# Kernel tuning notes

Hardware: AMD Instinct MI355X
Metric: run time of the kernel (lower is better)

The kernel has to match this reference:

```python
import jax, jax.numpy as jnp
import numpy as np

V, E, H = 348, 512, 1024  # vocab, embed dim, GRU hidden


def gru_cell(x, h, w_ih, w_hh, b_ih, b_hh):
    # PyTorch GRUCell: gates ordered [r, z, n] along the 3H axis
    gi = x @ w_ih.T + b_ih            # [B, 3H]
    gh = h @ w_hh.T + b_hh            # [B, 3H]
    i_r, i_z, i_n = jnp.split(gi, 3, axis=-1)
    h_r, h_z, h_n = jnp.split(gh, 3, axis=-1)
    r = jax.nn.sigmoid(i_r + h_r)
    z = jax.nn.sigmoid(i_z + h_z)
    n = jnp.tanh(i_n + r * h_n)
    return (1.0 - z) * n + z * h


def setup_inputs() -> dict:
    key = jax.random.key(0)
    ks = jax.random.split(key, 20)
    B, T = 256, 128
    p = lambda k, shape: jax.random.normal(k, shape, dtype=jnp.float32) * 0.02
    return {
        "target": jax.random.randint(ks[0], (B, T), 0, V, dtype=jnp.int32),
        "bos": 1,
        "emb": p(ks[1], (V, E)),
        "w_ih1": p(ks[2], (3 * H, E)),  "w_hh1": p(ks[3], (3 * H, H)),
        "b_ih1": p(ks[4], (3 * H,)),    "b_hh1": p(ks[5], (3 * H,)),
        "w_ih2": p(ks[6], (3 * H, H)),  "w_hh2": p(ks[7], (3 * H, H)),
        "b_ih2": p(ks[8], (3 * H,)),    "b_hh2": p(ks[9], (3 * H,)),
        "w_ih3": p(ks[10], (3 * H, H)), "w_hh3": p(ks[11], (3 * H, H)),
        "b_ih3": p(ks[12], (3 * H,)),   "b_hh3": p(ks[13], (3 * H,)),
        "w_out": p(ks[14], (V, H)),     "b_out": p(ks[15], (V,)),
    }


def reference(target, bos, emb, w_ih1, w_hh1, b_ih1, b_hh1,
              w_ih2, w_hh2, b_ih2, b_hh2,
              w_ih3, w_hh3, b_ih3, b_hh3, w_out, b_out):
    B, T = target.shape
    # input tokens = [<bos>, target[:, :-1]]
    x_in = jnp.concatenate(
        [jnp.full((B, 1), bos, dtype=target.dtype), target[:, :-1]], axis=1)
    h0 = jnp.zeros((B, H), jnp.float32)
    lp0 = jnp.zeros((B,), jnp.float32)

    def step(carry, xt):
        h1, h2, h3, lp = carry
        tok, tgt = xt                     # [B], [B]
        e = emb[tok]                      # [B, E]
        h1 = gru_cell(e, h1, w_ih1, w_hh1, b_ih1, b_hh1)
        h2 = gru_cell(h1, h2, w_ih2, w_hh2, b_ih2, b_hh2)
        h3 = gru_cell(h2, h3, w_ih3, w_hh3, b_ih3, b_hh3)
        logits = h3 @ w_out.T + b_out     # [B, V]
        logp = jax.nn.log_softmax(logits, axis=-1)
        # NLLLoss in source = sum(one_hot(tgt) * log_prob) = gathered log-prob
        lp = lp + jnp.take_along_axis(logp, tgt[:, None], axis=1)[:, 0]
        return (h1, h2, h3, lp), None

    (_, _, _, log_probs), _ = jax.lax.scan(
        step, (h0, h0, h0, lp0), (x_in.T, target.T))
    return log_probs
```

## Files before the change

### kernel.cpp

```cpp
#include <hip/hip_runtime.h>
#include <hip/hip_bf16.h>
#include <cstdint>

constexpr int kT = 128;
constexpr int kB = 256;
constexpr int kE = 512;
constexpr int kH = 1024;
constexpr int kV = 348;
constexpr int kNG = 3072;
constexpr int NB = 208;

constexpr float kScale = 32.f;
constexpr float kInvSS = 1.f / 1024.f;

typedef float f4v __attribute__((ext_vector_type(4)));
typedef unsigned short u16;
typedef unsigned char u8;

__device__ __forceinline__ u8 f2e4m3(float x) {
  int p = __builtin_amdgcn_cvt_pk_fp8_f32(x, x, 0, false);
  return (u8)(p & 0xff);
}

__device__ __forceinline__ uint64_t ldv_u64(const void* p) {
  return __hip_atomic_load((const uint64_t*)p, __ATOMIC_RELAXED, __HIP_MEMORY_SCOPE_AGENT);
}
__device__ __forceinline__ void stv_u8(u8* p, u8 v) {
  __hip_atomic_store(p, v, __ATOMIC_RELAXED, __HIP_MEMORY_SCOPE_AGENT);
}

__device__ __forceinline__ int permn(int n) {
  int gate = n >> 10, j = n & 1023;
  return ((j >> 4) * 48) + gate * 16 + (j & 15);
}

struct Params {
  const int* target; const int* bosp; const float* b_out;
  const u8 *w1i, *w1h, *w2i, *w2h, *w3i, *w3h, *wout, *embb;
  const float *bi1, *bh1, *bi2, *bh2, *bi3, *bh3;
  float *h1f, *h2f, *h3f;
  u8    *h1b, *h2b, *h3b;
  float *lp;
  unsigned *acnt; unsigned *gflag;
};

union SMem {
  struct { u8 A[128 * 128]; u8 B[96 * 128]; } mm;
  float logits[16 * 400];
};

__device__ __forceinline__ void gbar(unsigned* acnt, unsigned* gflag, unsigned s) {
  asm volatile("s_waitcnt vmcnt(0)" ::: "memory");
  __syncthreads();
  if (threadIdx.x == 0) {
    const unsigned g = blockIdx.x & 31u;
    __hip_atomic_fetch_add(&acnt[g * 16], 1u, __ATOMIC_RELAXED, __HIP_MEMORY_SCOPE_AGENT);
    if (blockIdx.x == 0) {
      for (;;) {
        unsigned sum = 0;
#pragma unroll
        for (int i = 0; i < 32; ++i)
          sum += __hip_atomic_load(&acnt[i * 16], __ATOMIC_RELAXED, __HIP_MEMORY_SCOPE_AGENT);
        if (sum >= (unsigned)NB * (s + 1u)) break;
        __builtin_amdgcn_s_sleep(4);
      }
#pragma unroll
      for (int i = 0; i < 32; ++i)
        __hip_atomic_store(&gflag[i * 16], s + 1u, __ATOMIC_RELAXED, __HIP_MEMORY_SCOPE_AGENT);
    } else {
      while (__hip_atomic_load(&gflag[g * 16], __ATOMIC_RELAXED, __HIP_MEMORY_SCOPE_AGENT) <= s)
        __builtin_amdgcn_s_sleep(8);
    }
    asm volatile("" ::: "memory");
  }
  __syncthreads();
}

template<int K, bool EMB>
__device__ __forceinline__ void mm_phase(SMem& sm, const u8* __restrict__ Asrc,
    const u8* __restrict__ W, int b0, int n0,
    f4v* aR, f4v* aZ, f4v* aN,
    const int* __restrict__ target, int bos, int u)
{
  const int t = threadIdx.x, lane = t & 63, wv = t >> 6;
  const int wm = wv >> 1, wg = wv & 1, li = lane & 15, q = lane >> 4;
  uint64_t ra[4][2];
  uint4 rb[3];

  auto stage = [&](int k0) {
#pragma unroll
    for (int p = 0; p < 4; ++p) {
      int id = p * 256 + t, r = id >> 3, c = id & 7;
      if (EMB) {
        int tok = (u == 0) ? bos : target[(b0 + r) * kT + (u - 1)];
        uint4 v = *(const uint4*)&Asrc[(size_t)tok * K + k0 + c * 16];
        ra[p][0] = ((uint64_t)v.y << 32) | v.x;
        ra[p][1] = ((uint64_t)v.w << 32) | v.z;
      } else {
        const u8* src = Asrc + (size_t)(b0 + r) * kH + k0 + c * 16;
        ra[p][0] = ldv_u64(src); ra[p][1] = ldv_u64(src + 8);
      }
    }
#pragma unroll
    for (int p = 0; p < 3; ++p) {
      int id = p * 256 + t, r = id >> 3, c = id & 7;
      rb[p] = *(const uint4*)&W[(size_t)(n0 + r) * K + k0 + c * 16];
    }
  };

  stage(0);
  for (int it = 0; it < K / 128; ++it) {
    __syncthreads();
#pragma unroll
    for (int p = 0; p < 4; ++p) {
      int id = p * 256 + t, r = id >> 3, c = id & 7;
      const int u0 = c * 2, rx = r & 15;
      u8* base = &sm.mm.A[r * 128];
      *(uint64_t*)(base + 8 * (u0 ^ rx)) = ra[p][0];
      *(uint64_t*)(base + 8 * ((u0 + 1) ^ rx)) = ra[p][1];
    }
#pragma unroll
    for (int p = 0; p < 3; ++p) {
      int id = p * 256 + t, r = id >> 3, c = id & 7;
      const int u0 = c * 2, rx = r & 15;
      u8* base = &sm.mm.B[r * 128];
      *(uint64_t*)(base + 8 * (u0 ^ rx)) = (uint64_t)rb[p].x | ((uint64_t)rb[p].y << 32);
      *(uint64_t*)(base + 8 * ((u0 + 1) ^ rx)) = (uint64_t)rb[p].z | ((uint64_t)rb[p].w << 32);
    }
    __syncthreads();
    if (it + 1 < K / 128) stage((it + 1) * 128);
#pragma unroll
    for (int kk = 0; kk < 128; kk += 32) {
      const int swz = 8 * (((kk >> 3) + q) ^ li);
      long a[4], bb[3];
#pragma unroll
      for (int m2 = 0; m2 < 4; ++m2)
        a[m2] = *(const long*)&sm.mm.A[(64 * wm + 16 * m2 + li) * 128 + swz];
#pragma unroll
      for (int g = 0; g < 3; ++g)
        bb[g] = *(const long*)&sm.mm.B[(48 * wg + 16 * g + li) * 128 + swz];
#pragma unroll
      for (int m2 = 0; m2 < 4; ++m2) {
        aR[m2] = __builtin_amdgcn_mfma_f32_16x16x32_fp8_fp8(a[m2], bb[0], aR[m2], 0, 0, 0);
        aZ[m2] = __builtin_amdgcn_mfma_f32_16x16x32_fp8_fp8(a[m2], bb[1], aZ[m2], 0, 0, 0);
        aN[m2] = __builtin_amdgcn_mfma_f32_16x16x32_fp8_fp8(a[m2], bb[2], aN[m2], 0, 0, 0);
      }
    }
  }
}

template<int K1, bool L1>
__device__ void do_L(SMem& sm, const u8* __restrict__ xsrc,
                     const u8* __restrict__ hbPrev, const float* __restrict__ hfPrev,
                     const u8* __restrict__ Wih, const u8* __restrict__ Whh,
                     const float* __restrict__ biP, const float* __restrict__ bhP,
                     float* __restrict__ hfOut, u8* __restrict__ hbOut,
                     const int* __restrict__ target, int bos, int u, int mt, int jt)
{
  const int b0 = mt * 128, j0 = jt * 32, n0 = jt * 96;
  f4v aR[4], aZ[4], aNi[4], aNh[4];
#pragma unroll
  for (int i = 0; i < 4; ++i) {
    aR[i] = f4v{0.f,0.f,0.f,0.f}; aZ[i] = f4v{0.f,0.f,0.f,0.f};
    aNi[i] = f4v{0.f,0.f,0.f,0.f}; aNh[i] = f4v{0.f,0.f,0.f,0.f};
  }
  mm_phase<K1, L1>(sm, xsrc, Wih, b0, n0, aR, aZ, aNi, target, bos, u);
  mm_phase<kH, false>(sm, hbPrev, Whh, b0, n0, aR, aZ, aNh, target, bos, u);

  const int t = threadIdx.x, lane = t & 63, wv = t >> 6;
  const int wm = wv >> 1, wg = wv & 1, li = lane & 15, q = lane >> 4;
  const int j = j0 + 16 * wg + li;
  const int cr = n0 + 48 * wg + li;
  const float bR = biP[cr] + bhP[cr];
  const float bZ = biP[cr + 16] + bhP[cr + 16];
  const float biN = biP[cr + 32], bhN = bhP[cr + 32];
  float hold[4][4];
#pragma unroll
  for (int m2 = 0; m2 < 4; ++m2)
#pragma unroll
    for (int r = 0; r < 4; ++r) {
      int b = b0 + 64 * wm + 16 * m2 + 4 * q + r;
      hold[m2][r] = hfPrev[(size_t)b * kH + j];
    }
#pragma unroll
  for (int m2 = 0; m2 < 4; ++m2)
#pragma unroll
    for (int r = 0; r < 4; ++r) {
      int b = b0 + 64 * wm + 16 * m2 + 4 * q + r;
      float rg = 1.f / (1.f + __expf(-(aR[m2][r] * kInvSS + bR)));
      float zg = 1.f / (1.f + __expf(-(aZ[m2][r] * kInvSS + bZ)));
      float np = (aNi[m2][r] * kInvSS + biN) + rg * (aNh[m2][r] * kInvSS + bhN);
      float nh = 2.f / (1.f + __expf(-2.f * np)) - 1.f;
      float hnew = (1.f - zg) * nh + zg * hold[m2][r];
      hfOut[(size_t)b * kH + j] = hnew;
      stv_u8(&hbOut[(size_t)b * kH + j], f2e4m3(hnew * kScale));
    }
}

__device__ void do_E(SMem& sm, const u8* __restrict__ h3b, const u8* __restrict__ wo,
                     const float* __restrict__ b_out, const int* __restrict__ target,
                     float* __restrict__ lp, int u, int tile)
{
  const int b0 = tile * 16;
  const int t = threadIdx.x, lane = t & 63, wv = t >> 6;
  const int li = lane & 15, q = lane >> 4;
  f4v acc[6];
#pragma unroll
  for (int f = 0; f < 6; ++f) acc[f] = f4v{0.f, 0.f, 0.f, 0.f};

  const u8* ap = h3b + (size_t)(b0 + li) * kH + q * 8;
  uint64_t aCur = ldv_u64(ap);
  uint64_t bCur[6], bNx[6];
#pragma unroll
  for (int f = 0; f < 6; ++f)
    bCur[f] = *(const uint64_t*)&wo[(size_t)(96 * wv + 16 * f + li) * kH + q * 8];
  for (int k0 = 0; k0 < kH; k0 += 32) {
    uint64_t aNx = 0;
    if (k0 + 32 < kH) {
      aNx = ldv_u64(ap + k0 + 32);
#pragma unroll
      for (int f = 0; f < 6; ++f)
        bNx[f] = *(const uint64_t*)&wo[(size_t)(96 * wv + 16 * f + li) * kH + k0 + 32 + q * 8];
    }
#pragma unroll
    for (int f = 0; f < 6; ++f)
      acc[f] = __builtin_amdgcn_mfma_f32_16x16x32_fp8_fp8((long)aCur, (long)bCur[f], acc[f], 0, 0, 0);
    aCur = aNx;
#pragma unroll
    for (int f = 0; f < 6; ++f) bCur[f] = bNx[f];
  }
#pragma unroll
  for (int f = 0; f < 6; ++f) {
    int n = 96 * wv + 16 * f + li;
    if (n < kV) {
      float bo = b_out[n];
#pragma unroll
      for (int r = 0; r < 4; ++r)
        sm.logits[(4 * q + r) * 400 + n] = acc[f][r] * kInvSS + bo;
    }
  }
  __syncthreads();
  int m = 4 * wv + q;
  int b = b0 + m;
  float mx = -1e30f;
  for (int cc = li; cc < kV; cc += 16) mx = fmaxf(mx, sm.logits[m * 400 + cc]);
#pragma unroll
  for (int d = 1; d < 16; d <<= 1) mx = fmaxf(mx, __shfl_xor(mx, d, 16));
  float se = 0.f;
  for (int cc = li; cc < kV; cc += 16) se += __expf(sm.logits[m * 400 + cc] - mx);
#pragma unroll
  for (int d = 1; d < 16; d <<= 1) se += __shfl_xor(se, d, 16);
  int tgt = target[b * kT + u];
  float logp = sm.logits[m * 400 + tgt] - mx - __logf(se);
  if (li == 0) lp[b] += logp;
}

__global__ __launch_bounds__(256, 1) void rnn_main(Params P)
{
  __shared__ SMem sm;
  const int bid = blockIdx.x;
  const int bos = P.bosp[0];
  const size_t HS = (size_t)kB * kH;

  const int local = bid & 63;
  const int mt = (local >> 3) & 1;
  const int jt = (local & 7) | ((local >> 4) << 3);

  for (int s = 0; s < kT + 3; ++s) {
    if (bid < 64) {
      int u = s;
      if (u < kT)
        do_L<kE, true>(sm, P.embb,
                       P.h1b + (size_t)((u - 1) & 1) * HS, P.h1f + (size_t)((u - 1) & 1) * HS,
                       P.w1i, P.w1h, P.bi1, P.bh1,
                       P.h1f + (size_t)(u & 1) * HS, P.h1b + (size_t)(u & 1) * HS,
                       P.target, bos, u, mt, jt);
    } else if (bid < 128) {
      int u = s - 1;
      if (u >= 0 && u < kT)
        do_L<kH, false>(sm, P.h1b + (size_t)(u & 1) * HS,
                        P.h2b + (size_t)((u - 1) & 1) * HS, P.h2f + (size_t)((u - 1) & 1) * HS,
                        P.w2i, P.w2h, P.bi2, P.bh2,
                        P.h2f + (size_t)(u & 1) * HS, P.h2b + (size_t)(u & 1) * HS,
                        P.target, bos, u, mt, jt);
    } else if (bid < 192) {
      int u = s - 2;
      if (u >= 0 && u < kT)
        do_L<kH, false>(sm, P.h2b + (size_t)(u & 1) * HS,
                        P.h3b + (size_t)((u - 1) & 1) * HS, P.h3f + (size_t)((u - 1) & 1) * HS,
                        P.w3i, P.w3h, P.bi3, P.bh3,
                        P.h3f + (size_t)(u & 1) * HS, P.h3b + (size_t)(u & 1) * HS,
                        P.target, bos, u, mt, jt);
    } else {
      int u = s - 3;
      if (u >= 0 && u < kT)
        do_E(sm, P.h3b + (size_t)(u & 1) * HS, P.wout, P.b_out, P.target, P.lp, u, bid - 192);
    }
    gbar(P.acnt, P.gflag, (unsigned)s);
  }
}

__global__ void k_conv_w(const float* __restrict__ w, u8* __restrict__ wp, int K, int logK) {
  int idx = blockIdx.x * 256 + threadIdx.x;
  if (idx >= kNG * K) return;
  int n = idx >> logK, k = idx & (K - 1);
  wp[(size_t)permn(n) * K + k] = f2e4m3(w[idx] * kScale);
}
__global__ void k_conv_b(const float* __restrict__ b, float* __restrict__ bp) {
  int idx = blockIdx.x * 256 + threadIdx.x;
  if (idx < kNG) bp[permn(idx)] = b[idx];
}
__global__ void k_conv_wout(const float* __restrict__ w, u8* __restrict__ wp) {
  int idx = blockIdx.x * 256 + threadIdx.x;
  if (idx >= 384 * kH) return;
  int n = idx >> 10, k = idx & 1023;
  wp[idx] = (n < kV) ? f2e4m3(w[(size_t)n * kH + k] * kScale) : (u8)0;
}
__global__ void k_conv_emb(const float* __restrict__ e, u8* __restrict__ ep) {
  int idx = blockIdx.x * 256 + threadIdx.x;
  if (idx < kV * kE) ep[idx] = f2e4m3(e[idx] * kScale);
}

extern "C" void kernel_launch(void* const* d_in, const int* in_sizes, int n_in,
                              void* d_out, int out_size, void* d_ws, size_t ws_size,
                              hipStream_t stream)
{
  const int*   target = (const int*)d_in[0];
  const int*   bosp   = (const int*)d_in[1];
  const float* emb    = (const float*)d_in[2];
  const float* w_ih1  = (const float*)d_in[3];
  const float* w_hh1  = (const float*)d_in[4];
  const float* b_ih1  = (const float*)d_in[5];
  const float* b_hh1  = (const float*)d_in[6];
  const float* w_ih2  = (const float*)d_in[7];
  const float* w_hh2  = (const float*)d_in[8];
  const float* b_ih2  = (const float*)d_in[9];
  const float* b_hh2  = (const float*)d_in[10];
  const float* w_ih3  = (const float*)d_in[11];
  const float* w_hh3  = (const float*)d_in[12];
  const float* b_ih3  = (const float*)d_in[13];
  const float* b_hh3  = (const float*)d_in[14];
  const float* w_out  = (const float*)d_in[15];
  const float* b_out  = (const float*)d_in[16];

  char* ws = (char*)d_ws;
  size_t off = 0;
  auto alloc = [&](size_t bytes) -> void* {
    void* p = ws + off;
    off = (off + bytes + 511) & ~(size_t)511;
    return p;
  };
  u8* w1i = (u8*)alloc((size_t)kNG * kE);
  u8* w1h = (u8*)alloc((size_t)kNG * kH);
  u8* w2i = (u8*)alloc((size_t)kNG * kH);
  u8* w2h = (u8*)alloc((size_t)kNG * kH);
  u8* w3i = (u8*)alloc((size_t)kNG * kH);
  u8* w3h = (u8*)alloc((size_t)kNG * kH);
  u8* wo  = (u8*)alloc((size_t)384 * kH);
  u8* eb  = (u8*)alloc((size_t)kV * kE);
  float* bi1 = (float*)alloc(kNG * 4);
  float* bh1 = (float*)alloc(kNG * 4);
  float* bi2 = (float*)alloc(kNG * 4);
  float* bh2 = (float*)alloc(kNG * 4);
  float* bi3 = (float*)alloc(kNG * 4);
  float* bh3 = (float*)alloc(kNG * 4);
  float* h1f = (float*)alloc((size_t)2 * kB * kH * 4);
  float* h2f = (float*)alloc((size_t)2 * kB * kH * 4);
  float* h3f = (float*)alloc((size_t)2 * kB * kH * 4);
  u8* h1b = (u8*)alloc((size_t)2 * kB * kH);
  u8* h2b = (u8*)alloc((size_t)2 * kB * kH);
  u8* h3b = (u8*)alloc((size_t)2 * kB * kH);
  unsigned* bar = (unsigned*)alloc(4096);
  (void)ws_size; (void)in_sizes; (void)n_in; (void)out_size;

  k_conv_w<<<(kNG * kE + 255) / 256, 256, 0, stream>>>(w_ih1, w1i, kE, 9);
  k_conv_w<<<(kNG * kH + 255) / 256, 256, 0, stream>>>(w_hh1, w1h, kH, 10);
  k_conv_w<<<(kNG * kH + 255) / 256, 256, 0, stream>>>(w_ih2, w2i, kH, 10);
  k_conv_w<<<(kNG * kH + 255) / 256, 256, 0, stream>>>(w_hh2, w2h, kH, 10);
  k_conv_w<<<(kNG * kH + 255) / 256, 256, 0, stream>>>(w_ih3, w3i, kH, 10);
  k_conv_w<<<(kNG * kH + 255) / 256, 256, 0, stream>>>(w_hh3, w3h, kH, 10);
  k_conv_b<<<(kNG + 255) / 256, 256, 0, stream>>>(b_ih1, bi1);
  k_conv_b<<<(kNG + 255) / 256, 256, 0, stream>>>(b_hh1, bh1);
  k_conv_b<<<(kNG + 255) / 256, 256, 0, stream>>>(b_ih2, bi2);
  k_conv_b<<<(kNG + 255) / 256, 256, 0, stream>>>(b_hh2, bh2);
  k_conv_b<<<(kNG + 255) / 256, 256, 0, stream>>>(b_ih3, bi3);
  k_conv_b<<<(kNG + 255) / 256, 256, 0, stream>>>(b_hh3, bh3);
  k_conv_wout<<<(384 * kH + 255) / 256, 256, 0, stream>>>(w_out, wo);
  k_conv_emb<<<(kV * kE + 255) / 256, 256, 0, stream>>>(emb, eb);

  hipMemsetAsync(h1f, 0, (size_t)3 * 2 * kB * kH * 4, stream);
  hipMemsetAsync(h1b, 0, (size_t)3 * 2 * kB * kH, stream);
  hipMemsetAsync(bar, 0, 4096, stream);
  hipMemsetAsync(d_out, 0, (size_t)kB * 4, stream);

  Params P;
  P.target = target; P.bosp = bosp; P.b_out = b_out;
  P.w1i = w1i; P.w1h = w1h; P.w2i = w2i; P.w2h = w2h; P.w3i = w3i; P.w3h = w3h;
  P.wout = wo; P.embb = eb;
  P.bi1 = bi1; P.bh1 = bh1; P.bi2 = bi2; P.bh2 = bh2; P.bi3 = bi3; P.bh3 = bh3;
  P.h1f = h1f; P.h2f = h2f; P.h3f = h3f;
  P.h1b = h1b; P.h2b = h2b; P.h3b = h3b;
  P.lp = (float*)d_out;
  P.acnt = bar; P.gflag = bar + 512;

  rnn_main<<<dim3(NB), dim3(256), 0, stream>>>(P);
}
```

Baseline: 4.038 ms.

## Decentralize grid barrier and prefetch hidden-state tiles ahead of matmul phases

The grid barrier no longer funnels through block 0 broadcasting a flag. Every block's leader now polls the 32 arrival counters itself, which removes one hop of cross-CU latency per step but raises atomic polling traffic. do_L issues the first hidden-state A-tile loads before the input-weight phase so their latency overlaps that phase. do_E loads its whole 1024-byte A row up front into registers and fully unrolls the K loop, which raises register pressure.

Measured after the change: 8.674 ms. +114.8%, slower.

```diff
diff --git a/kernel.cpp b/kernel.cpp
--- a/kernel.cpp
+++ b/kernel.cpp
@@ -41,7 +41,7 @@
   float *h1f, *h2f, *h3f;
   u8    *h1b, *h2b, *h3b;
   float *lp;
-  unsigned *acnt; unsigned *gflag;
+  unsigned *acnt;
 };
 
 union SMem {
@@ -49,45 +49,38 @@
   float logits[16 * 400];
 };
 
-__device__ __forceinline__ void gbar(unsigned* acnt, unsigned* gflag, unsigned s) {
+__device__ __forceinline__ void gbar(unsigned* acnt, unsigned s) {
   asm volatile("s_waitcnt vmcnt(0)" ::: "memory");
   __syncthreads();
   if (threadIdx.x == 0) {
     const unsigned g = blockIdx.x & 31u;
     __hip_atomic_fetch_add(&acnt[g * 16], 1u, __ATOMIC_RELAXED, __HIP_MEMORY_SCOPE_AGENT);
-    if (blockIdx.x == 0) {
-      for (;;) {
-        unsigned sum = 0;
-#pragma unroll
-        for (int i = 0; i < 32; ++i)
-          sum += __hip_atomic_load(&acnt[i * 16], __ATOMIC_RELAXED, __HIP_MEMORY_SCOPE_AGENT);
-        if (sum >= (unsigned)NB * (s + 1u)) break;
-        __builtin_amdgcn_s_sleep(4);
-      }
+    for (;;) {
+      unsigned sum = 0;
 #pragma unroll
       for (int i = 0; i < 32; ++i)
-        __hip_atomic_store(&gflag[i * 16], s + 1u, __ATOMIC_RELAXED, __HIP_MEMORY_SCOPE_AGENT);
-    } else {
-      while (__hip_atomic_load(&gflag[g * 16], __ATOMIC_RELAXED, __HIP_MEMORY_SCOPE_AGENT) <= s)
-        __builtin_amdgcn_s_sleep(8);
+        sum += __hip_atomic_load(&acnt[i * 16], __ATOMIC_RELAXED, __HIP_MEMORY_SCOPE_AGENT);
+      if (sum >= (unsigned)NB * (s + 1u)) break;
+      __builtin_amdgcn_s_sleep(4);
     }
     asm volatile("" ::: "memory");
   }
   __syncthreads();
 }
 
-template<int K, bool EMB>
+template<int K, bool EMB, bool APRE>
 __device__ __forceinline__ void mm_phase(SMem& sm, const u8* __restrict__ Asrc,
     const u8* __restrict__ W, int b0, int n0,
     f4v* aR, f4v* aZ, f4v* aN,
-    const int* __restrict__ target, int bos, int u)
+    const int* __restrict__ target, int bos, int u,
+    const uint64_t (*preA)[2])
 {
   const int t = threadIdx.x, lane = t & 63, wv = t >> 6;
   const int wm = wv >> 1, wg = wv & 1, li = lane & 15, q = lane >> 4;
   uint64_t ra[4][2];
   uint4 rb[3];
 
-  auto stage = [&](int k0) {
+  auto stageA = [&](int k0) {
 #pragma unroll
     for (int p = 0; p < 4; ++p) {
       int id = p * 256 + t, r = id >> 3, c = id & 7;
@@ -101,6 +94,8 @@
         ra[p][0] = ldv_u64(src); ra[p][1] = ldv_u64(src + 8);
       }
     }
+  };
+  auto stageB = [&](int k0) {
 #pragma unroll
     for (int p = 0; p < 3; ++p) {
       int id = p * 256 + t, r = id >> 3, c = id & 7;
@@ -108,7 +103,13 @@
     }
   };
 
-  stage(0);
+  if constexpr (APRE) {
+#pragma unroll
+    for (int p = 0; p < 4; ++p) { ra[p][0] = preA[p][0]; ra[p][1] = preA[p][1]; }
+  } else {
+    stageA(0);
+  }
+  stageB(0);
   for (int it = 0; it < K / 128; ++it) {
     __syncthreads();
 #pragma unroll
@@ -128,7 +129,7 @@
       *(uint64_t*)(base + 8 * ((u0 + 1) ^ rx)) = (uint64_t)rb[p].z | ((uint64_t)rb[p].w << 32);
     }
     __syncthreads();
-    if (it + 1 < K / 128) stage((it + 1) * 128);
+    if (it + 1 < K / 128) { stageA((it + 1) * 128); stageB((it + 1) * 128); }
 #pragma unroll
     for (int kk = 0; kk < 128; kk += 32) {
       const int swz = 8 * (((kk >> 3) + q) ^ li);
@@ -149,7 +150,7 @@
   }
 }
 
-template<int K1, bool L1>
+template<int K1, bool L1f>
 __device__ void do_L(SMem& sm, const u8* __restrict__ xsrc,
                      const u8* __restrict__ hbPrev, const float* __restrict__ hfPrev,
                      const u8* __restrict__ Wih, const u8* __restrict__ Whh,
@@ -158,16 +159,26 @@
                      const int* __restrict__ target, int bos, int u, int mt, int jt)
 {
   const int b0 = mt * 128, j0 = jt * 32, n0 = jt * 96;
+  const int t = threadIdx.x;
+
+  uint64_t preA[4][2];
+#pragma unroll
+  for (int p = 0; p < 4; ++p) {
+    int id = p * 256 + t, r = id >> 3, c = id & 7;
+    const u8* src = hbPrev + (size_t)(b0 + r) * kH + c * 16;
+    preA[p][0] = ldv_u64(src); preA[p][1] = ldv_u64(src + 8);
+  }
+
   f4v aR[4], aZ[4], aNi[4], aNh[4];
 #pragma unroll
   for (int i = 0; i < 4; ++i) {
     aR[i] = f4v{0.f,0.f,0.f,0.f}; aZ[i] = f4v{0.f,0.f,0.f,0.f};
     aNi[i] = f4v{0.f,0.f,0.f,0.f}; aNh[i] = f4v{0.f,0.f,0.f,0.f};
   }
-  mm_phase<K1, L1>(sm, xsrc, Wih, b0, n0, aR, aZ, aNi, target, bos, u);
-  mm_phase<kH, false>(sm, hbPrev, Whh, b0, n0, aR, aZ, aNh, target, bos, u);
-
-  const int t = threadIdx.x, lane = t & 63, wv = t >> 6;
+  mm_phase<K1, L1f, false>(sm, xsrc, Wih, b0, n0, aR, aZ, aNi, target, bos, u, nullptr);
+  mm_phase<kH, false, true>(sm, hbPrev, Whh, b0, n0, aR, aZ, aNh, target, bos, u, preA);
+
+  const int lane = t & 63, wv = t >> 6;
   const int wm = wv >> 1, wg = wv & 1, li = lane & 15, q = lane >> 4;
   const int j = j0 + 16 * wg + li;
   const int cr = n0 + 48 * wg + li;
@@ -209,25 +220,29 @@
   for (int f = 0; f < 6; ++f) acc[f] = f4v{0.f, 0.f, 0.f, 0.f};
 
   const u8* ap = h3b + (size_t)(b0 + li) * kH + q * 8;
-  uint64_t aCur = ldv_u64(ap);
-  uint64_t bCur[6], bNx[6];
-#pragma unroll
-  for (int f = 0; f < 6; ++f)
-    bCur[f] = *(const uint64_t*)&wo[(size_t)(96 * wv + 16 * f + li) * kH + q * 8];
-  for (int k0 = 0; k0 < kH; k0 += 32) {
-    uint64_t aNx = 0;
-    if (k0 + 32 < kH) {
-      aNx = ldv_u64(ap + k0 + 32);
+  uint64_t aAll[32];
+#pragma unroll
+  for (int k = 0; k < 32; ++k) aAll[k] = ldv_u64(ap + k * 32);
+
+  const u8* wp = wo + (size_t)(96 * wv + li) * kH + q * 8;
+  uint64_t bC[6];
+#pragma unroll
+  for (int f = 0; f < 6; ++f) bC[f] = *(const uint64_t*)(wp + (size_t)16 * f * kH);
+#pragma unroll
+  for (int k0 = 0; k0 < 32; ++k0) {
+    uint64_t bN[6];
+    if (k0 + 1 < 32) {
 #pragma unroll
       for (int f = 0; f < 6; ++f)
-        bNx[f] = *(const uint64_t*)&wo[(size_t)(96 * wv + 16 * f + li) * kH + k0 + 32 + q * 8];
+        bN[f] = *(const uint64_t*)(wp + (size_t)16 * f * kH + (k0 + 1) * 32);
     }
 #pragma unroll
     for (int f = 0; f < 6; ++f)
-      acc[f] = __builtin_amdgcn_mfma_f32_16x16x32_fp8_fp8((long)aCur, (long)bCur[f], acc[f], 0, 0, 0);
-    aCur = aNx;
-#pragma unroll
-    for (int f = 0; f < 6; ++f) bCur[f] = bNx[f];
+      acc[f] = __builtin_amdgcn_mfma_f32_16x16x32_fp8_fp8((long)aAll[k0], (long)bC[f], acc[f], 0, 0, 0);
+    if (k0 + 1 < 32) {
+#pragma unroll
+      for (int f = 0; f < 6; ++f) bC[f] = bN[f];
+    }
   }
 #pragma unroll
   for (int f = 0; f < 6; ++f) {
@@ -296,7 +311,7 @@
       if (u >= 0 && u < kT)
         do_E(sm, P.h3b + (size_t)(u & 1) * HS, P.wout, P.b_out, P.target, P.lp, u, bid - 192);
     }
-    gbar(P.acnt, P.gflag, (unsigned)s);
+    gbar(P.acnt, (unsigned)s);
   }
 }
 
@@ -401,7 +416,7 @@
   P.h1f = h1f; P.h2f = h2f; P.h3f = h3f;
   P.h1b = h1b; P.h2b = h2b; P.h3b = h3b;
   P.lp = (float*)d_out;
-  P.acnt = bar; P.gflag = bar + 512;
+  P.acnt = bar;
 
   rnn_main<<<dim3(NB), dim3(256), 0, stream>>>(P);
 }
```
